# Optimization experiments

Measured on AMD Instinct MI355X. Metric: run time of the kernel, lower is better.

## Reference

```python
import jax, jax.numpy as jnp
import numpy as np

S, B, C = 7, 2, 20
N = B * 5 + C  # 30
L_COORD, L_NOOBJ = 5.0, 0.5


def setup_inputs() -> dict:
    key = jax.random.key(0)
    k1, k2, k3, k4 = jax.random.split(key, 4)
    batch = 16384
    pred = jax.random.uniform(k1, (batch, S, S, N), dtype=jnp.float32)
    target = jax.random.uniform(k2, (batch, S, S, N), dtype=jnp.float32)
    # rescale w/h channels of both boxes to [0.5, 1) so the (buggy) in-place
    # coordinate transform never yields negative values under sqrt
    wh_idx = jnp.array([2, 3, 7, 8])
    pred = pred.at[..., wh_idx].set(0.5 + 0.5 * pred[..., wh_idx])
    target = target.at[..., wh_idx].set(0.5 + 0.5 * target[..., wh_idx])
    obj = jax.random.uniform(k3, (batch, S, S)) < 0.25
    conf = 0.1 + 0.9 * jax.random.uniform(k4, (batch, S, S))
    target = target.at[..., 4].set(jnp.where(obj, conf, 0.0))
    return {"pred": pred, "target": target}


def _yolo_loss(pred, target):
    # Faithful vectorization of the original loop-y torch forward, bugs included:
    #  * x2y2 is computed from the ALREADY transformed xy (xy_new/S + 0.5*wh)
    #  * lambda_coord only multiplies the x / sqrt(w) terms, not y / sqrt(h)
    #  * the selected per-cell loss SUMS l1+l2+l3+IoU (IoU itself is added)
    #  * only the first min(S^2, #coord_cells) coord cells (global flatten
    #    order across the batch) contribute to bbox_loss
    #  * class-prob loss slices dim1 of a [M,2,5] tensor with 10: -> empty -> 0
    p = pred.reshape(-1, N)   # [M, 30], M = b*S*S, row-major like torch mask gather
    t = target.reshape(-1, N)
    obj = t[:, 4] > 0
    rank = jnp.cumsum(obj.astype(jnp.int32)) - 1  # rank among coord cells
    active = obj & (rank < S * S)                 # cells whose bbox loss counts

    pb = p[:, :10].reshape(-1, B, 5)  # [M, B, 5]
    tb = t[:, :10].reshape(-1, B, 5)

    def transform(box):
        xy = box[..., :2] / S - 0.5 * box[..., 2:4]      # new x1,y1
        x2y2 = xy / S + 0.5 * box[..., 2:4]              # uses NEW xy (original bug)
        return xy, x2y2

    pxy, p2 = transform(pb)
    txy, t2 = transform(tb)

    l1 = L_COORD * (txy[..., 0] - pxy[..., 0]) ** 2 + (txy[..., 1] - pxy[..., 1]) ** 2
    l2 = (L_COORD * (jnp.sqrt(t2[..., 0]) - jnp.sqrt(p2[..., 0])) ** 2
          + (jnp.sqrt(t2[..., 1]) - jnp.sqrt(p2[..., 1])) ** 2)
    l3 = (tb[..., 4] - pb[..., 4]) ** 2

    # IoU between pred box j and target box j (boxes as [x1,y1,x2,y2])
    lt = jnp.maximum(pxy, txy)
    rb = jnp.minimum(p2, t2)
    wh = jnp.maximum(rb - lt, 0.0)
    inter = wh[..., 0] * wh[..., 1]
    area_p = (p2[..., 0] - pxy[..., 0]) * (p2[..., 1] - pxy[..., 1])
    area_t = (t2[..., 0] - txy[..., 0]) * (t2[..., 1] - txy[..., 1])
    iou = inter / (area_p + area_t - inter)  # [M, B]

    tot = l1 + l2 + l3 + iou                 # sum(info[argmax]) includes IoU
    jstar = jnp.argmax(iou, axis=1)          # responsible box per cell
    sel = jnp.take_along_axis(tot, jstar[:, None], axis=1)[:, 0]
    bbox_loss = jnp.sum(jnp.where(active, sel, 0.0))

    # no-object confidence loss over both boxes' conf channels (4 and 9)
    noobj = ~obj
    conf_sq = (p[:, 4] - t[:, 4]) ** 2 + (p[:, 9] - t[:, 9]) ** 2
    noobj_loss = L_NOOBJ * jnp.sum(jnp.where(noobj, conf_sq, 0.0))

    # class prob loss: original slices [:, 10:] on a [M, B, 5] tensor -> empty -> 0
    class_prob_loss = jnp.float32(0.0)

    return bbox_loss + noobj_loss + class_prob_loss


def reference(pred, target):
    return _yolo_loss(pred, target)
```

## Files before the change

kernel.cpp:

```cpp
#include <hip/hip_runtime.h>

#define NCH 30
#define RANK_LIMIT 49
#define L_COORD 5.0f
#define L_NOOBJ 0.5f

#define NB 980
#define UNROLL 8
#define OUTER 3

__global__ __launch_bounds__(256) void noobj_kernel(const float4* __restrict__ pv,
                                                    const float4* __restrict__ tv,
                                                    const float* __restrict__ ts,
                                                    float* __restrict__ ws) {
    float acc = 0.0f;
    int base = blockIdx.x * (256 * UNROLL) + threadIdx.x;
    const int step = NB * 256 * UNROLL;

    for (int outer = 0; outer < OUTER; ++outer, base += step) {
        float4 vp[UNROLL], vt[UNROLL];
        float  gate[UNROLL];
        int    kk[UNROLL];

        #pragma unroll
        for (int u = 0; u < UNROLL; ++u) {
            int i = base + u * 256;
            vp[u] = pv[i];
            vt[u] = tv[i];
        }
        #pragma unroll
        for (int u = 0; u < UNROLL; ++u) {
            int i = base + u * 256;
            int pair = i / 15;
            int k = i - pair * 15;
            kk[u] = k;
            gate[u] = 1.0f;
            if (k == 2)      gate[u] = ts[pair * 60 + 4];
            else if (k == 9) gate[u] = ts[pair * 60 + 34];
        }
        #pragma unroll
        for (int u = 0; u < UNROLL; ++u) {
            int k = kk[u];
            if (k == 1) {
                float t4 = vt[u].x;
                if (!(t4 > 0.0f)) { float d = vp[u].x - t4; acc += d * d; }
            } else if (k == 2) {
                if (!(gate[u] > 0.0f)) { float d = vp[u].y - vt[u].y; acc += d * d; }
            } else if (k == 8) {
                float t4 = vt[u].z;
                if (!(t4 > 0.0f)) { float d = vp[u].z - t4; acc += d * d; }
            } else if (k == 9) {
                if (!(gate[u] > 0.0f)) { float d = vp[u].w - vt[u].w; acc += d * d; }
            }
        }
    }

    #pragma unroll
    for (int off = 32; off > 0; off >>= 1)
        acc += __shfl_down(acc, off, 64);
    __shared__ float s[4];
    int lane = threadIdx.x & 63;
    int wid  = threadIdx.x >> 6;
    if (lane == 0) s[wid] = acc;
    __syncthreads();
    if (threadIdx.x == 0)
        ws[blockIdx.x] = s[0] + s[1] + s[2] + s[3];
}

__device__ inline float sel_loss(const float* __restrict__ p,
                                 const float* __restrict__ t, int row) {
    const float invS = 1.0f / 7.0f;
    int b0 = row * NCH;
    float tot0 = 0.f, tot1 = 0.f, iou0 = 0.f, iou1 = 0.f;
    #pragma unroll
    for (int j = 0; j < 2; ++j) {
        int o = b0 + 5 * j;
        float px = p[o + 0], py = p[o + 1], pw = p[o + 2], ph = p[o + 3], pc = p[o + 4];
        float tx = t[o + 0], ty = t[o + 1], tw = t[o + 2], th = t[o + 3], tc = t[o + 4];
        float pxy0 = px * invS - 0.5f * pw;
        float pxy1 = py * invS - 0.5f * ph;
        float p2x  = pxy0 * invS + 0.5f * pw;
        float p2y  = pxy1 * invS + 0.5f * ph;
        float txy0 = tx * invS - 0.5f * tw;
        float txy1 = ty * invS - 0.5f * th;
        float t2x  = txy0 * invS + 0.5f * tw;
        float t2y  = txy1 * invS + 0.5f * th;
        float d0 = txy0 - pxy0, d1 = txy1 - pxy1;
        float l1 = L_COORD * d0 * d0 + d1 * d1;
        float s0 = sqrtf(t2x) - sqrtf(p2x);
        float s1 = sqrtf(t2y) - sqrtf(p2y);
        float l2 = L_COORD * s0 * s0 + s1 * s1;
        float dc = tc - pc;
        float l3 = dc * dc;
        float ltx = fmaxf(pxy0, txy0), lty = fmaxf(pxy1, txy1);
        float rbx = fminf(p2x, t2x),   rby = fminf(p2y, t2y);
        float wx  = fmaxf(rbx - ltx, 0.0f);
        float wy  = fmaxf(rby - lty, 0.0f);
        float inter  = wx * wy;
        float area_p = (p2x - pxy0) * (p2y - pxy1);
        float area_t = (t2x - txy0) * (t2y - txy1);
        float io = inter / (area_p + area_t - inter);
        float tt = l1 + l2 + l3 + io;
        if (j == 0) { iou0 = io; tot0 = tt; }
        else        { iou1 = io; tot1 = tt; }
    }
    return (iou1 > iou0) ? tot1 : tot0;
}

__global__ __launch_bounds__(256) void bbox_kernel(const float* __restrict__ p,
                                                   const float* __restrict__ t,
                                                   const float* __restrict__ ws,
                                                   float* __restrict__ out, int M) {
    __shared__ int   s_wcnt[4];
    __shared__ int   s_base;
    __shared__ float s_part[4];
    if (threadIdx.x == 0) s_base = 0;
    __syncthreads();

    float local = 0.0f;
    for (int start = 0; start < M; start += 256) {
        int row = start + (int)threadIdx.x;
        bool obj = false;
        if (row < M) obj = t[row * NCH + 4] > 0.0f;

        unsigned long long mask = __ballot(obj);
        int lane = threadIdx.x & 63;
        int wid  = threadIdx.x >> 6;
        if (lane == 0) s_wcnt[wid] = __popcll(mask);
        __syncthreads();

        int base = s_base;
        int off = 0;
        for (int w = 0; w < wid; ++w) off += s_wcnt[w];
        int rank = base + off + __popcll(mask & ((1ULL << lane) - 1ULL));
        if (obj && rank < RANK_LIMIT) local += sel_loss(p, t, row);
        __syncthreads();

        if (threadIdx.x == 0)
            s_base = base + s_wcnt[0] + s_wcnt[1] + s_wcnt[2] + s_wcnt[3];
        __syncthreads();
        if (s_base >= RANK_LIMIT) break;
    }

    for (int i = threadIdx.x; i < NB; i += 256)
        local += L_NOOBJ * ws[i];

    #pragma unroll
    for (int o = 32; o > 0; o >>= 1)
        local += __shfl_down(local, o, 64);
    int lane = threadIdx.x & 63;
    int wid  = threadIdx.x >> 6;
    if (lane == 0) s_part[wid] = local;
    __syncthreads();
    if (threadIdx.x == 0)
        out[0] = s_part[0] + s_part[1] + s_part[2] + s_part[3];
}

extern "C" void kernel_launch(void* const* d_in, const int* in_sizes, int n_in,
                              void* d_out, int out_size, void* d_ws, size_t ws_size,
                              hipStream_t stream) {
    const float* pred = (const float*)d_in[0];
    const float* targ = (const float*)d_in[1];
    float* out = (float*)d_out;
    float* partials = (float*)d_ws;

    int M = in_sizes[0] / NCH;

    noobj_kernel<<<NB, 256, 0, stream>>>((const float4*)pred, (const float4*)targ,
                                         targ, partials);
    bbox_kernel<<<1, 256, 0, stream>>>(pred, targ, partials, out, M);
}
```

Before: 209.9 us.

## Split target gating into separate kernel producing compact gate buffer

Adds a gate_kernel that streams the full target tensor and writes only the four needed confidence values per row pair into a compact workspace buffer. The noobj kernel then streams only pred plus that small gate buffer, using a flat, one-pass grid of 4704 blocks with 5 strided float4 loads per thread instead of the earlier outer loop. The target is still read in full, so total DRAM traffic stays about the same and a small gate write plus an extra kernel launch are added. It also relies on the workspace being large enough to hold the gate buffer.

```diff
diff --git a/kernel.cpp b/kernel.cpp
--- a/kernel.cpp
+++ b/kernel.cpp
@@ -5,53 +5,61 @@
 #define L_COORD 5.0f
 #define L_NOOBJ 0.5f
 
-#define NB 980
-#define UNROLL 8
-#define OUTER 3
+#define NF4 6021120
+#define NB 4704
+#define UNROLL 5
+#define STRIDE (NB * 256)
+
+#define GATE_OFF_FLOATS 16384
+
+__global__ __launch_bounds__(256) void gate_kernel(const float4* __restrict__ tv,
+                                                   float* __restrict__ gate) {
+    int gid = blockIdx.x * 256 + threadIdx.x;
+    float4 v[UNROLL];
+    #pragma unroll
+    for (int u = 0; u < UNROLL; ++u)
+        v[u] = tv[gid + u * STRIDE];
+    #pragma unroll
+    for (int u = 0; u < UNROLL; ++u) {
+        int i = gid + u * STRIDE;
+        int pair = i / 15;
+        int k = i - pair * 15;
+        int g = 4 * pair;
+        if (k == 1)      gate[g + 0] = v[u].x;
+        else if (k == 2) gate[g + 1] = v[u].y;
+        else if (k == 8) gate[g + 2] = v[u].z;
+        else if (k == 9) gate[g + 3] = v[u].w;
+    }
+}
 
 __global__ __launch_bounds__(256) void noobj_kernel(const float4* __restrict__ pv,
-                                                    const float4* __restrict__ tv,
-                                                    const float* __restrict__ ts,
-                                                    float* __restrict__ ws) {
+                                                    const float* __restrict__ gate,
+                                                    float* __restrict__ partials) {
+    int gid = blockIdx.x * 256 + threadIdx.x;
+    float4 v[UNROLL];
+    #pragma unroll
+    for (int u = 0; u < UNROLL; ++u)
+        v[u] = pv[gid + u * STRIDE];
+
     float acc = 0.0f;
-    int base = blockIdx.x * (256 * UNROLL) + threadIdx.x;
-    const int step = NB * 256 * UNROLL;
-
-    for (int outer = 0; outer < OUTER; ++outer, base += step) {
-        float4 vp[UNROLL], vt[UNROLL];
-        float  gate[UNROLL];
-        int    kk[UNROLL];
-
-        #pragma unroll
-        for (int u = 0; u < UNROLL; ++u) {
-            int i = base + u * 256;
-            vp[u] = pv[i];
-            vt[u] = tv[i];
-        }
-        #pragma unroll
-        for (int u = 0; u < UNROLL; ++u) {
-            int i = base + u * 256;
-            int pair = i / 15;
-            int k = i - pair * 15;
-            kk[u] = k;
-            gate[u] = 1.0f;
-            if (k == 2)      gate[u] = ts[pair * 60 + 4];
-            else if (k == 9) gate[u] = ts[pair * 60 + 34];
-        }
-        #pragma unroll
-        for (int u = 0; u < UNROLL; ++u) {
-            int k = kk[u];
-            if (k == 1) {
-                float t4 = vt[u].x;
-                if (!(t4 > 0.0f)) { float d = vp[u].x - t4; acc += d * d; }
-            } else if (k == 2) {
-                if (!(gate[u] > 0.0f)) { float d = vp[u].y - vt[u].y; acc += d * d; }
-            } else if (k == 8) {
-                float t4 = vt[u].z;
-                if (!(t4 > 0.0f)) { float d = vp[u].z - t4; acc += d * d; }
-            } else if (k == 9) {
-                if (!(gate[u] > 0.0f)) { float d = vp[u].w - vt[u].w; acc += d * d; }
-            }
+    #pragma unroll
+    for (int u = 0; u < UNROLL; ++u) {
+        int i = gid + u * STRIDE;
+        int pair = i / 15;
+        int k = i - pair * 15;
+        int g = 4 * pair;
+        if (k == 1) {
+            float t4 = gate[g + 0];
+            if (!(t4 > 0.0f)) { float d = v[u].x - t4; acc += d * d; }
+        } else if (k == 2) {
+            float t4 = gate[g + 0];
+            if (!(t4 > 0.0f)) { float d = v[u].y - gate[g + 1]; acc += d * d; }
+        } else if (k == 8) {
+            float t4 = gate[g + 2];
+            if (!(t4 > 0.0f)) { float d = v[u].z - t4; acc += d * d; }
+        } else if (k == 9) {
+            float t4 = gate[g + 2];
+            if (!(t4 > 0.0f)) { float d = v[u].w - gate[g + 3]; acc += d * d; }
         }
     }
 
@@ -64,7 +72,7 @@
     if (lane == 0) s[wid] = acc;
     __syncthreads();
     if (threadIdx.x == 0)
-        ws[blockIdx.x] = s[0] + s[1] + s[2] + s[3];
+        partials[blockIdx.x] = s[0] + s[1] + s[2] + s[3];
 }
 
 __device__ inline float sel_loss(const float* __restrict__ p,
@@ -109,7 +117,7 @@
 
 __global__ __launch_bounds__(256) void bbox_kernel(const float* __restrict__ p,
                                                    const float* __restrict__ t,
-                                                   const float* __restrict__ ws,
+                                                   const float* __restrict__ partials,
                                                    float* __restrict__ out, int M) {
     __shared__ int   s_wcnt[4];
     __shared__ int   s_base;
@@ -143,7 +151,7 @@
     }
 
     for (int i = threadIdx.x; i < NB; i += 256)
-        local += L_NOOBJ * ws[i];
+        local += L_NOOBJ * partials[i];
 
     #pragma unroll
     for (int o = 32; o > 0; o >>= 1)
@@ -163,10 +171,11 @@
     const float* targ = (const float*)d_in[1];
     float* out = (float*)d_out;
     float* partials = (float*)d_ws;
+    float* gate = (float*)d_ws + GATE_OFF_FLOATS;
 
     int M = in_sizes[0] / NCH;
 
-    noobj_kernel<<<NB, 256, 0, stream>>>((const float4*)pred, (const float4*)targ,
-                                         targ, partials);
+    gate_kernel<<<NB, 256, 0, stream>>>((const float4*)targ, gate);
+    noobj_kernel<<<NB, 256, 0, stream>>>((const float4*)pred, gate, partials);
     bbox_kernel<<<1, 256, 0, stream>>>(pred, targ, partials, out, M);
 }
```

New measurement: 226.8 us. +8.0%, slower.

## Use nontemporal loads, wider grid, and shuffle-based gate lookup in noobj kernel

Applied to the files above, without the earlier changes.

Replaces the per-thread outer loop with a single pass over more blocks (5880 blocks × 4 float4s per thread). Loads now use nontemporal builtins. The gate value for the second conf channel comes from the neighbouring lane's float4 via shfl_up, with a global-memory fallback only for lane 0. The per-channel branching becomes branchless selects. The aim is to cut scattered gate loads and branch divergence and to stream data past the cache. In exchange there are more partials for the single-block bbox kernel to reduce.

```diff
diff --git a/kernel.cpp b/kernel.cpp
--- a/kernel.cpp
+++ b/kernel.cpp
@@ -5,66 +5,65 @@
 #define L_COORD 5.0f
 #define L_NOOBJ 0.5f
 
-#define NB 980
-#define UNROLL 8
-#define OUTER 3
+#define NB 5880
+#define UNROLL 4
 
-__global__ __launch_bounds__(256) void noobj_kernel(const float4* __restrict__ pv,
-                                                    const float4* __restrict__ tv,
+typedef float vfloat4 __attribute__((ext_vector_type(4)));
+
+__global__ __launch_bounds__(256) void noobj_kernel(const vfloat4* __restrict__ pv,
+                                                    const vfloat4* __restrict__ tv,
                                                     const float* __restrict__ ts,
-                                                    float* __restrict__ ws) {
+                                                    float* __restrict__ partials) {
+    const int tid  = threadIdx.x;
+    const int lane = tid & 63;
+    const int base = blockIdx.x * (256 * UNROLL) + tid;
+
+    vfloat4 vp[UNROLL], vt[UNROLL];
+    #pragma unroll
+    for (int u = 0; u < UNROLL; ++u) {
+        int i = base + u * 256;
+        vp[u] = __builtin_nontemporal_load(&pv[i]);
+        vt[u] = __builtin_nontemporal_load(&tv[i]);
+    }
+
     float acc = 0.0f;
-    int base = blockIdx.x * (256 * UNROLL) + threadIdx.x;
-    const int step = NB * 256 * UNROLL;
+    #pragma unroll
+    for (int u = 0; u < UNROLL; ++u) {
+        int i = base + u * 256;
+        int pair = i / 15;
+        int k = i - pair * 15;
 
-    for (int outer = 0; outer < OUTER; ++outer, base += step) {
-        float4 vp[UNROLL], vt[UNROLL];
-        float  gate[UNROLL];
-        int    kk[UNROLL];
+        float gx = __shfl_up(vt[u].x, 1, 64);
+        float gz = __shfl_up(vt[u].z, 1, 64);
+        if (lane == 0) {
+            if (k == 2) gx = ts[pair * 60 + 4];
+            if (k == 9) gz = ts[pair * 60 + 34];
+        }
 
-        #pragma unroll
-        for (int u = 0; u < UNROLL; ++u) {
-            int i = base + u * 256;
-            vp[u] = pv[i];
-            vt[u] = tv[i];
-        }
-        #pragma unroll
-        for (int u = 0; u < UNROLL; ++u) {
-            int i = base + u * 256;
-            int pair = i / 15;
-            int k = i - pair * 15;
-            kk[u] = k;
-            gate[u] = 1.0f;
-            if (k == 2)      gate[u] = ts[pair * 60 + 4];
-            else if (k == 9) gate[u] = ts[pair * 60 + 34];
-        }
-        #pragma unroll
-        for (int u = 0; u < UNROLL; ++u) {
-            int k = kk[u];
-            if (k == 1) {
-                float t4 = vt[u].x;
-                if (!(t4 > 0.0f)) { float d = vp[u].x - t4; acc += d * d; }
-            } else if (k == 2) {
-                if (!(gate[u] > 0.0f)) { float d = vp[u].y - vt[u].y; acc += d * d; }
-            } else if (k == 8) {
-                float t4 = vt[u].z;
-                if (!(t4 > 0.0f)) { float d = vp[u].z - t4; acc += d * d; }
-            } else if (k == 9) {
-                if (!(gate[u] > 0.0f)) { float d = vp[u].w - vt[u].w; acc += d * d; }
-            }
-        }
+        float d1 = vp[u].x - vt[u].x;
+        float d2 = vp[u].y - vt[u].y;
+        float d8 = vp[u].z - vt[u].z;
+        float d9 = vp[u].w - vt[u].w;
+
+        float c1 = (!(vt[u].x > 0.0f)) ? d1 * d1 : 0.0f;
+        float c2 = (!(gx      > 0.0f)) ? d2 * d2 : 0.0f;
+        float c8 = (!(vt[u].z > 0.0f)) ? d8 * d8 : 0.0f;
+        float c9 = (!(gz      > 0.0f)) ? d9 * d9 : 0.0f;
+
+        float contrib = (k == 1) ? c1 : (k == 2) ? c2 : (k == 8) ? c8
+                      : (k == 9) ? c9 : 0.0f;
+        acc += contrib;
     }
 
     #pragma unroll
     for (int off = 32; off > 0; off >>= 1)
         acc += __shfl_down(acc, off, 64);
     __shared__ float s[4];
-    int lane = threadIdx.x & 63;
-    int wid  = threadIdx.x >> 6;
+    int wid = tid >> 6;
     if (lane == 0) s[wid] = acc;
     __syncthreads();
-    if (threadIdx.x == 0)
-        ws[blockIdx.x] = s[0] + s[1] + s[2] + s[3];
+    if (tid == 0)
+        partials[blockIdx.x] = s[0] + s[1] + s[2] + s[3];
 }
 
 __device__ inline float sel_loss(const float* __restrict__ p,
@@ -109,7 +108,7 @@
 
 __global__ __launch_bounds__(256) void bbox_kernel(const float* __restrict__ p,
                                                    const float* __restrict__ t,
-                                                   const float* __restrict__ ws,
+                                                   const float* __restrict__ partials,
                                                    float* __restrict__ out, int M) {
     __shared__ int   s_wcnt[4];
     __shared__ int   s_base;
@@ -143,7 +142,7 @@
     }
 
     for (int i = threadIdx.x; i < NB; i += 256)
-        local += L_NOOBJ * ws[i];
+        local += L_NOOBJ * partials[i];
 
     #pragma unroll
     for (int o = 32; o > 0; o >>= 1)
@@ -166,7 +165,7 @@
 
     int M = in_sizes[0] / NCH;
 
-    noobj_kernel<<<NB, 256, 0, stream>>>((const float4*)pred, (const float4*)targ,
+    noobj_kernel<<<NB, 256, 0, stream>>>((const vfloat4*)pred, (const vfloat4*)targ,
                                          targ, partials);
     bbox_kernel<<<1, 256, 0, stream>>>(pred, targ, partials, out, M);
 }
```

After: 197.0 us. 6.2% less time.
